# Performance work log

Measured on AMD Instinct MI355X. Metric: run time of the kernel, lower is better.

Reference implementation:

```python
import jax, jax.numpy as jnp
import numpy as np

B, T, D, H = 4, 2048, 1024, 16
DK, DV, CHUNK = D // H, 2 * D // H, 64  # head_k_dim=64, head_v_dim=128 (expand_v=2.0)
EPS = 1e-5


def setup_inputs() -> dict:
    key = jax.random.key(0)
    ks = jax.random.split(key, 6)
    s = 0.02
    return {
        "x": jax.random.normal(ks[0], (B, T, D), jnp.float32),
        "Wq": jax.random.normal(ks[1], (D, H * DK), jnp.float32) * s,
        "Wk": jax.random.normal(ks[2], (D, H * DK), jnp.float32) * s,
        "Wv": jax.random.normal(ks[3], (D, H * DV), jnp.float32) * s,
        "Wg": jax.random.normal(ks[4], (D, H * DV), jnp.float32) * s,
        "Wo": jax.random.normal(ks[5], (H * DV, D), jnp.float32) * s,
        "g_norm_w": jnp.ones((DV,), jnp.float32),
    }


def _rope(q):
    # q: [B, T, H, DK]; non-interleaved (rotate-half) rotary, base 10000
    half = DK // 2
    inv_freq = 1.0 / (10000.0 ** (jnp.arange(half, dtype=jnp.float32) / half))
    freqs = jnp.arange(T, dtype=jnp.float32)[:, None] * inv_freq  # [T, half]
    cos = jnp.cos(freqs)[None, :, None, :]
    sin = jnp.sin(freqs)[None, :, None, :]
    q1, q2 = q[..., :half], q[..., half:]
    return jnp.concatenate([q1 * cos - q2 * sin, q2 * cos + q1 * sin], axis=-1)


def reference(x, Wq, Wk, Wv, Wg, Wo, g_norm_w):
    q = _rope((x @ Wq).reshape(B, T, H, DK)) * (DK ** -0.5)
    k = _rope((x @ Wk).reshape(B, T, H, DK))
    v = (x @ Wv).reshape(B, T, H, DV)

    N = T // CHUNK
    def tochunks(t):  # [B,T,H,Dh] -> [N,B,H,C,Dh]
        return t.reshape(B, N, CHUNK, H, t.shape[-1]).transpose(1, 0, 3, 2, 4)
    qc, kc, vc = tochunks(q), tochunks(k), tochunks(v)

    # per-head RetNet decay: gamma_h = 1 - 2^{-5-h}
    gamma = 1.0 - jnp.exp2(-5.0 - jnp.arange(H, dtype=jnp.float32))  # [H]
    i = jnp.arange(CHUNK, dtype=jnp.float32)
    # intra-chunk decay mask D[h,i,j] = gamma^{i-j} for j<=i else 0
    Dmask = jnp.where(i[:, None] >= i[None, :],
                      gamma[:, None, None] ** (i[:, None] - i[None, :]), 0.0)  # [H,C,C]
    cross = gamma[:, None] ** (i + 1.0)          # [H,C] query decay vs prev state
    kdec = gamma[:, None] ** (CHUNK - 1.0 - i)   # [H,C] key decay into new state
    chunk_dec = gamma ** CHUNK                   # [H]

    def step(S, qkv):
        q_, k_, v_ = qkv  # [B,H,C,DK], [B,H,C,DK], [B,H,C,DV]
        attn = jnp.einsum('bhid,bhjd->bhij', q_, k_) * Dmask
        o = jnp.einsum('bhij,bhjv->bhiv', attn, v_)
        o = o + jnp.einsum('bhid,bhdv->bhiv', q_ * cross[None, :, :, None], S)
        S = S * chunk_dec[None, :, None, None] + \
            jnp.einsum('bhjd,bhjv->bhdv', k_ * kdec[None, :, :, None], v_)
        return S, o

    S0 = jnp.zeros((B, H, DK, DV), x.dtype)
    _, o = jax.lax.scan(step, S0, (qc, kc, vc))  # [N,B,H,C,DV]
    o = o.transpose(1, 0, 3, 2, 4).reshape(B, T, H, DV)

    # fused RMSNorm + swish gate (FusedRMSNormSwishGate)
    g = (x @ Wg).reshape(B, T, H, DV)
    o = o * jax.lax.rsqrt(jnp.mean(o * o, axis=-1, keepdims=True) + EPS) * g_norm_w
    o = o * (g * jax.nn.sigmoid(g))
    return o.reshape(B, T, H * DV) @ Wo
```

## Files before the change

kernel.cpp:

```cpp
#include <hip/hip_runtime.h>
#include <hip/hip_bf16.h>
#include <math.h>

typedef unsigned short u16;
typedef unsigned int u32;
typedef __attribute__((ext_vector_type(8))) short bf16x8;
typedef __attribute__((ext_vector_type(4))) float f32x4;


__device__ __forceinline__ u16 f2bf(float f) {
  union { float f; unsigned u; } a; a.f = f;
  unsigned u = a.u;
  unsigned r = (u + 0x7fffu + ((u >> 16) & 1u)) >> 16;
  return (u16)r;
}
__device__ __forceinline__ float bf2f(u16 s) {
  union { unsigned u; float f; } a; a.u = ((unsigned)s) << 16; return a.f;
}

__global__ void k_sentinel(float* out) {
  if (threadIdx.x == 0 && blockIdx.x == 0) out[0] = 1.0e6f;
}

__device__ __forceinline__ void split8r(const float* t, bf16x8& hi, bf16x8& lo) {
#pragma unroll
  for (int m = 0; m < 8; ++m) {
    union { float f; u32 u; } c; c.f = t[m];
    union { u32 u; float f; } hf; hf.u = c.u & 0xffff0000u;
    union { float f; u32 u; } lw; lw.f = t[m] - hf.f;
    hi[m] = (short)(u16)(c.u >> 16);
    lo[m] = (short)(u16)(lw.u >> 16);
  }
}
__device__ __forceinline__ void split8p(const float* __restrict__ p, bf16x8& hi, bf16x8& lo) {
  f32x4 a = *(const f32x4*)p;
  f32x4 b = *(const f32x4*)(p + 4);
  float t[8];
  t[0]=a[0]; t[1]=a[1]; t[2]=a[2]; t[3]=a[3]; t[4]=b[0]; t[5]=b[1]; t[6]=b[2]; t[7]=b[3];
  split8r(t, hi, lo);
}

__device__ __forceinline__ void bar_lds() {
  asm volatile("s_waitcnt lgkmcnt(0)" ::: "memory");
  __builtin_amdgcn_sched_barrier(0);
  __builtin_amdgcn_s_barrier();
}

__device__ __forceinline__ void gload16(const u16* g, u16* l) {
  __builtin_amdgcn_global_load_lds(
      (const __attribute__((address_space(1))) unsigned int*)g,
      (__attribute__((address_space(3))) unsigned int*)l, 16, 0, 0);
}

__global__ __launch_bounds__(256) void k_cvt_x(const float* __restrict__ src, u16* __restrict__ dst) {
  int i = blockIdx.x * 256 + threadIdx.x;
  float4 v = ((const float4*)src)[i];
  ushort4 o;
  o.x = f2bf(v.x); o.y = f2bf(v.y); o.z = f2bf(v.z); o.w = f2bf(v.w);
  ((ushort4*)dst)[i] = o;
}

__global__ __launch_bounds__(256) void k_ropetab(float2* __restrict__ tab) {
  int idx = blockIdx.x * 256 + threadIdx.x;
  int t = idx >> 5, i = idx & 31;
  float invf = powf(10000.f, -(float)i * (1.f / 32.f));
  float ang = (float)t * invf;
  float2 cs; cs.x = cosf(ang); cs.y = sinf(ang);
  tab[idx] = cs;
}

__global__ __launch_bounds__(256) void k_transpose_all(
    const float* __restrict__ Wq, const float* __restrict__ Wk, const float* __restrict__ Wv,
    const float* __restrict__ Wg, const float* __restrict__ Wo,
    u16* __restrict__ Wqkb, u16* __restrict__ Wvgb, u16* __restrict__ Wob) {
  int z = blockIdx.x;
  const float* src; u16* dst; int K, N, bx, by;
  if (z < 1024)      { src = Wq; dst = Wqkb;                       K = 1024; N = 1024; int r = z;        bx = r & 31; by = r >> 5; }
  else if (z < 2048) { src = Wk; dst = Wqkb + (size_t)1024 * 1024; K = 1024; N = 1024; int r = z - 1024; bx = r & 31; by = r >> 5; }
  else if (z < 4096) { src = Wv; dst = Wvgb;                       K = 1024; N = 2048; int r = z - 2048; bx = r & 63; by = r >> 6; }
  else if (z < 6144) { src = Wg; dst = Wvgb + (size_t)2048 * 1024; K = 1024; N = 2048; int r = z - 4096; bx = r & 63; by = r >> 6; }
  else               { src = Wo; dst = Wob;                        K = 2048; N = 1024; int r = z - 6144; bx = r & 31; by = r >> 5; }
  __shared__ float tile[32][33];
  int n0 = bx * 32, k0 = by * 32;
  int tx = threadIdx.x & 31, ty = threadIdx.x >> 5;
  for (int r = 0; r < 32; r += 8)
    tile[ty + r][tx] = src[(size_t)(k0 + ty + r) * N + n0 + tx];
  __syncthreads();
  for (int r = 0; r < 32; r += 8)
    dst[(size_t)(n0 + ty + r) * K + k0 + tx] = f2bf(tile[tx][ty + r]);
}

#define STG3(t, sl)                                                                  \
  {                                                                                  \
    _Pragma("unroll")                                                                \
    for (int q = 0; q < 2; ++q) {                                                    \
      int s = w * 2 + q;                                                             \
      int dByte = s * 1024 + lane * 16;                                              \
      int u = dByte ^ (((dByte >> 9) & 1) << 5);                                     \
      int row = u >> 6, cb = u & 63;                                                 \
      gload16(&A[(size_t)(i0 + row) * K + (t) * 32 + (cb >> 1)], &As[sl][s * 512]);  \
      gload16(&Bt[(size_t)(n0 + row) * K + (t) * 32 + (cb >> 1)], &Bs[sl][s * 512]); \
    }                                                                                \
  }

__global__ __launch_bounds__(256, 2) void k_gemm_qkvg(const u16* __restrict__ A, const u16* __restrict__ Bt,
                                                      float* __restrict__ qk, u16* __restrict__ vg,
                                                      const float2* __restrict__ tab, int K) {
  __shared__ __attribute__((aligned(16))) u16 As[3][128 * 32];
  __shared__ __attribute__((aligned(16))) u16 Bs[3][128 * 32];
  int id = blockIdx.y * 48 + blockIdx.x;
  int x = id & 7, loc = id >> 3;
  int bxg = loc / 48, rem = loc - bxg * 48;
  int by8 = rem / 6, bxi = rem - by8 * 6;
  int bx = bxg * 6 + bxi, by = x * 8 + by8;
  int i0 = by * 128, n0 = bx * 128;
  int tid = threadIdx.x;
  int lane = tid & 63, w = tid >> 6;
  int wr = (w >> 1) * 64, wc = (w & 1) * 64;
  f32x4 acc[4][4];
#pragma unroll
  for (int m = 0; m < 4; ++m)
#pragma unroll
    for (int n = 0; n < 4; ++n) acc[m][n] = (f32x4){0.f, 0.f, 0.f, 0.f};
  int fr = lane & 15, kq = lane >> 4;
  int nkt = K >> 5;

  STG3(0, 0);
  STG3(1, 1);
  for (int t = 0; t < nkt; ++t) {
    if (t < nkt - 1) asm volatile("s_waitcnt vmcnt(4)" ::: "memory");
    else             asm volatile("s_waitcnt vmcnt(0)" ::: "memory");
    asm volatile("s_waitcnt lgkmcnt(0)" ::: "memory");
    __builtin_amdgcn_sched_barrier(0);
    __builtin_amdgcn_s_barrier();
    if (t + 2 < nkt) STG3(t + 2, (t + 2) % 3);
    int cur = t % 3;
    bf16x8 af[4], bfr[4];
#pragma unroll
    for (int m = 0; m < 4; ++m) {
      int rr = wr + m * 16 + fr;
      int idx = (rr * 32 + kq * 8) ^ (((rr >> 3) & 1) << 4);
      af[m] = *(const bf16x8*)&As[cur][idx];
    }
#pragma unroll
    for (int n = 0; n < 4; ++n) {
      int rr = wc + n * 16 + fr;
      int idx = (rr * 32 + kq * 8) ^ (((rr >> 3) & 1) << 4);
      bfr[n] = *(const bf16x8*)&Bs[cur][idx];
    }
    __builtin_amdgcn_s_setprio(1);
#pragma unroll
    for (int m = 0; m < 4; ++m)
#pragma unroll
      for (int n = 0; n < 4; ++n)
        acc[m][n] = __builtin_amdgcn_mfma_f32_16x16x32_bf16(af[m], bfr[n], acc[m][n], 0, 0, 0);
    __builtin_amdgcn_s_setprio(0);
  }

  int rb = (lane >> 4) * 4, cb2 = lane & 15;
  if (n0 < 2048) {
    float scale = (n0 < 1024) ? 0.125f : 1.0f;
#pragma unroll
    for (int m = 0; m < 4; ++m)
#pragma unroll
      for (int n = 0; n < 2; ++n) {
        int gc = n0 + wc + n * 16 + cb2;
        int ii = n * 16 + cb2;
#pragma unroll
        for (int r = 0; r < 4; ++r) {
          int gr = i0 + wr + m * 16 + rb + r;
          int t = gr & 2047;
          float2 cs = tab[t * 32 + ii];
          float q1 = acc[m][n][r], q2 = acc[m][n + 2][r];
          qk[(size_t)gr * 2048 + gc]      = (q1 * cs.x - q2 * cs.y) * scale;
          qk[(size_t)gr * 2048 + gc + 32] = (q2 * cs.x + q1 * cs.y) * scale;
        }
      }
  } else {
#pragma unroll
    for (int m = 0; m < 4; ++m)
#pragma unroll
      for (int n = 0; n < 4; ++n) {
        int gr = i0 + wr + m * 16 + rb;
        int gc = n0 - 2048 + wc + n * 16 + cb2;
#pragma unroll
        for (int r = 0; r < 4; ++r)
          vg[(size_t)(gr + r) * 4096 + gc] = f2bf(acc[m][n][r]);
      }
  }
}

__global__ __launch_bounds__(256, 2) void k_gemm_out(const u16* __restrict__ A, const u16* __restrict__ Bt,
                                                     float* __restrict__ Cv, int N, int K) {
  __shared__ __attribute__((aligned(16))) u16 As[3][128 * 32];
  __shared__ __attribute__((aligned(16))) u16 Bs[3][128 * 32];
  int nbx = gridDim.x;
  int id = blockIdx.y * nbx + blockIdx.x;
  int cpx = (nbx * gridDim.y) >> 3;
  int sw = (id & 7) * cpx + (id >> 3);
  int bx = sw % nbx, by = sw / nbx;
  int i0 = by * 128, n0 = bx * 128;
  int tid = threadIdx.x;
  int lane = tid & 63, w = tid >> 6;
  int wr = (w >> 1) * 64, wc = (w & 1) * 64;
  f32x4 acc[4][4];
#pragma unroll
  for (int m = 0; m < 4; ++m)
#pragma unroll
    for (int n = 0; n < 4; ++n) acc[m][n] = (f32x4){0.f, 0.f, 0.f, 0.f};
  int fr = lane & 15, kq = lane >> 4;
  int nkt = K >> 5;

  STG3(0, 0);
  STG3(1, 1);
  for (int t = 0; t < nkt; ++t) {
    if (t < nkt - 1) asm volatile("s_waitcnt vmcnt(4)" ::: "memory");
    else             asm volatile("s_waitcnt vmcnt(0)" ::: "memory");
    asm volatile("s_waitcnt lgkmcnt(0)" ::: "memory");
    __builtin_amdgcn_sched_barrier(0);
    __builtin_amdgcn_s_barrier();
    if (t + 2 < nkt) STG3(t + 2, (t + 2) % 3);
    int cur = t % 3;
    bf16x8 af[4], bfr[4];
#pragma unroll
    for (int m = 0; m < 4; ++m) {
      int rr = wr + m * 16 + fr;
      int idx = (rr * 32 + kq * 8) ^ (((rr >> 3) & 1) << 4);
      af[m] = *(const bf16x8*)&As[cur][idx];
    }
#pragma unroll
    for (int n = 0; n < 4; ++n) {
      int rr = wc + n * 16 + fr;
      int idx = (rr * 32 + kq * 8) ^ (((rr >> 3) & 1) << 4);
      bfr[n] = *(const bf16x8*)&Bs[cur][idx];
    }
    __builtin_amdgcn_s_setprio(1);
#pragma unroll
    for (int m = 0; m < 4; ++m)
#pragma unroll
      for (int n = 0; n < 4; ++n)
        acc[m][n] = __builtin_amdgcn_mfma_f32_16x16x32_bf16(af[m], bfr[n], acc[m][n], 0, 0, 0);
    __builtin_amdgcn_s_setprio(0);
  }

  int rb = (lane >> 4) * 4, cb2 = lane & 15;
#pragma unroll
  for (int m = 0; m < 4; ++m)
#pragma unroll
    for (int n = 0; n < 4; ++n) {
      int gr = i0 + wr + m * 16 + rb;
      int gc = n0 + wc + n * 16 + cb2;
#pragma unroll
      for (int r = 0; r < 4; ++r)
        Cv[(size_t)(gr + r) * N + gc] = acc[m][n][r];
    }
}

__global__ __launch_bounds__(512) void k_retention(const float* __restrict__ qk, const u16* __restrict__ vg,
                                                   const float* __restrict__ gnw, u16* __restrict__ og) {
  int bh = blockIdx.x & 63, rq = blockIdx.x >> 6;
  int h = bh & 15, b = bh >> 4;
  int gi0 = rq * 16;

  __shared__ __attribute__((aligned(16))) float qs[16][68];
  __shared__ __attribute__((aligned(16))) float ks[64][68];
  __shared__ __attribute__((aligned(16))) u16 vst[128][88];
  __shared__ __attribute__((aligned(16))) u16 kta_h[8][520];
  __shared__ __attribute__((aligned(16))) u16 kta_l[8][520];
  __shared__ __attribute__((aligned(16))) u16 pa_h[16][68];
  __shared__ __attribute__((aligned(16))) u16 pa_l[16][68];
  __shared__ __attribute__((aligned(16))) u16 sst_h[8][1040];
  __shared__ __attribute__((aligned(16))) u16 sst_l[8][1040];
  __shared__ float dpow[72];
  __shared__ float ssred[8][16];

  int tid = threadIdx.x;
  int w = tid >> 6, l = tid & 63;
  int fr = l & 15, fq = l >> 4;
  float gamma = 1.f - exp2f(-5.f - (float)h);
  if (tid <= 64) dpow[tid] = powf(gamma, (float)tid);
  for (int c = tid; c < 4160; c += 512) { ((u32*)sst_h)[c] = 0; ((u32*)sst_l)[c] = 0; }
  __syncthreads();
  float cdec = dpow[64];

  int e0 = w * 16;
  float gww = gnw[e0 + fr];
  int khmax = (rq < 2) ? 1 : 2;

  int qi = tid >> 4, qd4 = (tid & 15) * 4;
  int sj = tid >> 3, sdg = (tid & 7) * 8;
  int vjp = tid & 31, ve8 = (tid >> 5) * 8;

  f32x4 Sacc[4][2];
#pragma unroll
  for (int dt = 0; dt < 4; ++dt)
#pragma unroll
    for (int nt = 0; nt < 2; ++nt) Sacc[dt][nt] = (f32x4){0.f, 0.f, 0.f, 0.f};

  f32x4 pq = (f32x4){0.f, 0.f, 0.f, 0.f};
  f32x4 pk0, pk1;
  bf16x8 pva, pvb;
  {
    int rowbase = b * 2048;
    if (tid < 256) pq = *(const f32x4*)&qk[(size_t)(rowbase + gi0 + qi) * 2048 + h * 64 + qd4];
    const float* kr = &qk[(size_t)(rowbase + sj) * 2048 + 1024 + h * 64 + sdg];
    pk0 = *(const f32x4*)kr;
    pk1 = *(const f32x4*)(kr + 4);
    const u16* vr = &vg[(size_t)(rowbase + 2 * vjp) * 4096 + h * 128 + ve8];
    pva = *(const bf16x8*)vr;
    pvb = *(const bf16x8*)(vr + 4096);
  }

  for (int n = 0; n < 32; ++n) {
    int rowbase = b * 2048 + n * 64;
    if (tid < 256) *(f32x4*)&qs[qi][qd4] = pq;
    {
      *(f32x4*)&ks[sj][sdg] = pk0;
      *(f32x4*)&ks[sj][sdg + 4] = pk1;
      float kdv = dpow[63 - sj];
      float kd[8];
#pragma unroll
      for (int m = 0; m < 4; ++m) { kd[m] = pk0[m] * kdv; kd[m + 4] = pk1[m] * kdv; }
      bf16x8 kh8, kl8;
      split8r(kd, kh8, kl8);
      int J = sj >> 3, s = sj & 7, dh = tid & 7;
#pragma unroll
      for (int m = 0; m < 8; ++m) {
        int blk = (dh * 8) | (m ^ dh);
        kta_h[J][blk * 8 + s] = (u16)kh8[m];
        kta_l[J][blk * 8 + s] = (u16)kl8[m];
      }
#pragma unroll
      for (int m = 0; m < 8; ++m)
        *(u32*)&vst[ve8 + m][2 * vjp] = (u32)(u16)pva[m] | ((u32)(u16)pvb[m] << 16);
    }
    __syncthreads();
    if (n < 31) {
      int rb2 = rowbase + 64;
      if (tid < 256) pq = *(const f32x4*)&qk[(size_t)(rb2 + gi0 + qi) * 2048 + h * 64 + qd4];
      const float* kr = &qk[(size_t)(rb2 + sj) * 2048 + 1024 + h * 64 + sdg];
      pk0 = *(const f32x4*)kr;
      pk1 = *(const f32x4*)(kr + 4);
      const u16* vr = &vg[(size_t)(rb2 + 2 * vjp) * 4096 + h * 128 + ve8];
      pva = *(const bf16x8*)vr;
      pvb = *(const bf16x8*)(vr + 4096);
    }
    bf16x8 qhc[2], qlc[2];
    split8p(&qs[fr][fq * 8], qhc[0], qlc[0]);
    split8p(&qs[fr][32 + fq * 8], qhc[1], qlc[1]);
    if (w < 4) {
      int ct = w;
      f32x4 at = (f32x4){0.f, 0.f, 0.f, 0.f};
      if (16 * ct <= gi0 + 15) {
#pragma unroll
        for (int kh = 0; kh < 2; ++kh) {
          bf16x8 kbh, kbl;
          split8p(&ks[16 * ct + fr][kh * 32 + fq * 8], kbh, kbl);
          at = __builtin_amdgcn_mfma_f32_16x16x32_bf16(kbh, qhc[kh], at, 0, 0, 0);
          at = __builtin_amdgcn_mfma_f32_16x16x32_bf16(kbl, qhc[kh], at, 0, 0, 0);
          at = __builtin_amdgcn_mfma_f32_16x16x32_bf16(kbh, qlc[kh], at, 0, 0, 0);
        }
      }
      int jb = 16 * ct + fq * 4;
      ushort4 wh, wl;
#pragma unroll
      for (int r = 0; r < 4; ++r) {
        int s = gi0 + fr - (jb + r);
        float val = (s >= 0) ? at[r] * dpow[s] : 0.f;
        union { float f; u32 u; } c; c.f = val;
        union { u32 u; float f; } hf; hf.u = c.u & 0xffff0000u;
        union { float f; u32 u; } lw; lw.f = val - hf.f;
        ((u16*)&wh)[r] = (u16)(c.u >> 16);
        ((u16*)&wl)[r] = (u16)(lw.u >> 16);
      }
      *(ushort4*)&pa_h[fr][jb] = wh;
      *(ushort4*)&pa_l[fr][jb] = wl;
    } else if (n < 31) {
      int eb = (w - 4) * 32;
#pragma unroll
      for (int dt = 0; dt < 4; ++dt)
#pragma unroll
        for (int nt = 0; nt < 2; ++nt)
#pragma unroll
          for (int r = 0; r < 4; ++r) Sacc[dt][nt][r] *= cdec;
      bf16x8 bv[2][2];
#pragma unroll
      for (int kh2 = 0; kh2 < 2; ++kh2)
#pragma unroll
        for (int nt = 0; nt < 2; ++nt)
          bv[kh2][nt] = *(const bf16x8*)&vst[eb + nt * 16 + fr][kh2 * 32 + fq * 8];
#pragma unroll
      for (int kh2 = 0; kh2 < 2; ++kh2) {
#pragma unroll
        for (int dt = 0; dt < 4; ++dt) {
          int d = dt * 16 + fr;
          int blk = d ^ ((dt * 2 + (fr >> 3)) & 7);
          bf16x8 ah = *(const bf16x8*)&kta_h[kh2 * 4 + fq][blk * 8];
          bf16x8 al = *(const bf16x8*)&kta_l[kh2 * 4 + fq][blk * 8];
#pragma unroll
          for (int nt = 0; nt < 2; ++nt) {
            Sacc[dt][nt] = __builtin_amdgcn_mfma_f32_16x16x32_bf16(ah, bv[kh2][nt], Sacc[dt][nt], 0, 0, 0);
            Sacc[dt][nt] = __builtin_amdgcn_mfma_f32_16x16x32_bf16(al, bv[kh2][nt], Sacc[dt][nt], 0, 0, 0);
          }
        }
      }
    }
    bar_lds();
    f32x4 o1 = (f32x4){0.f, 0.f, 0.f, 0.f};
    f32x4 o2 = (f32x4){0.f, 0.f, 0.f, 0.f};
#pragma unroll
    for (int kh2 = 0; kh2 < 2; ++kh2) {
      bf16x8 sh = *(const bf16x8*)&sst_h[kh2 * 4 + fq][(e0 + fr) * 8];
      bf16x8 sl = *(const bf16x8*)&sst_l[kh2 * 4 + fq][(e0 + fr) * 8];
      o2 = __builtin_amdgcn_mfma_f32_16x16x32_bf16(qhc[kh2], sh, o2, 0, 0, 0);
      o2 = __builtin_amdgcn_mfma_f32_16x16x32_bf16(qhc[kh2], sl, o2, 0, 0, 0);
      o2 = __builtin_amdgcn_mfma_f32_16x16x32_bf16(qlc[kh2], sh, o2, 0, 0, 0);
      if (kh2 < khmax) {
        bf16x8 ph = *(const bf16x8*)&pa_h[fr][kh2 * 32 + fq * 8];
        bf16x8 pl = *(const bf16x8*)&pa_l[fr][kh2 * 32 + fq * 8];
        bf16x8 bvv = *(const bf16x8*)&vst[e0 + fr][kh2 * 32 + fq * 8];
        o1 = __builtin_amdgcn_mfma_f32_16x16x32_bf16(ph, bvv, o1, 0, 0, 0);
        o1 = __builtin_amdgcn_mfma_f32_16x16x32_bf16(pl, bvv, o1, 0, 0, 0);
      }
    }
    float ofin[4], ssp[4];
#pragma unroll
    for (int r = 0; r < 4; ++r) {
      int gi = gi0 + fq * 4 + r;
      ofin[r] = o1[r] + dpow[gi + 1] * o2[r];
      ssp[r] = ofin[r] * ofin[r];
    }
#pragma unroll
    for (int r = 0; r < 4; ++r) {
      ssp[r] += __shfl_xor(ssp[r], 1, 64);
      ssp[r] += __shfl_xor(ssp[r], 2, 64);
      ssp[r] += __shfl_xor(ssp[r], 4, 64);
      ssp[r] += __shfl_xor(ssp[r], 8, 64);
    }
    if (fr == 0) {
#pragma unroll
      for (int r = 0; r < 4; ++r) ssred[w][fq * 4 + r] = ssp[r];
    }
    bar_lds();
#pragma unroll
    for (int r = 0; r < 4; ++r) {
      int i16 = fq * 4 + r;
      float tot = 0.f;
#pragma unroll
      for (int w2 = 0; w2 < 8; ++w2) tot += ssred[w2][i16];
      float rms = rsqrtf(tot * (1.f / 128.f) + 1e-5f);
      int grow = rowbase + gi0 + i16;
      float g = bf2f(vg[(size_t)grow * 4096 + 2048 + h * 128 + e0 + fr]);
      float y = ofin[r] * rms * gww * (g / (1.f + expf(-g)));
      og[(size_t)grow * 2048 + h * 128 + e0 + fr] = f2bf(y);
    }
    if (w >= 4 && n < 31) {
      int eb = (w - 4) * 32;
#pragma unroll
      for (int dt = 0; dt < 4; ++dt) {
        int g = dt * 2 + (fq >> 1);
#pragma unroll
        for (int nt = 0; nt < 2; ++nt) {
          int e = eb + nt * 16 + fr;
          ushort4 wh, wl;
#pragma unroll
          for (int r = 0; r < 4; ++r) {
            union { float f; u32 u; } c; c.f = Sacc[dt][nt][r];
            union { u32 u; float f; } hf; hf.u = c.u & 0xffff0000u;
            union { float f; u32 u; } lw; lw.f = Sacc[dt][nt][r] - hf.f;
            ((u16*)&wh)[r] = (u16)(c.u >> 16);
            ((u16*)&wl)[r] = (u16)(lw.u >> 16);
          }
          int idx = e * 8 + (fq & 1) * 4;
          *(ushort4*)&sst_h[g][idx] = wh;
          *(ushort4*)&sst_l[g][idx] = wl;
        }
      }
    }
  }
}

extern "C" void kernel_launch(void* const* d_in, const int* in_sizes, int n_in,
                              void* d_out, int out_size, void* d_ws, size_t ws_size,
                              hipStream_t stream) {
  const float* x   = (const float*)d_in[0];
  const float* Wq  = (const float*)d_in[1];
  const float* Wk  = (const float*)d_in[2];
  const float* Wv  = (const float*)d_in[3];
  const float* Wg  = (const float*)d_in[4];
  const float* Wo  = (const float*)d_in[5];
  const float* gnw = (const float*)d_in[6];
  float* out = (float*)d_out;

  const size_t MB = 1024 * 1024;
  char* ws = (char*)d_ws;
  u16*   xb   = (u16*)(ws + 0 * MB);
  u16*   Wqkb = (u16*)(ws + 16 * MB);
  u16*   Wvgb = (u16*)(ws + 20 * MB);
  float2* tab = (float2*)(ws + 28 * MB);
  float* qk   = (float*)(ws + 32 * MB);
  u16*   vg   = (u16*)(ws + 96 * MB);
  u16*   Wob  = (u16*)(ws + 160 * MB);
  u16*   og   = (u16*)(ws + 0 * MB);
  const size_t NEED = 164 * MB;
  if (ws_size < NEED) {
    k_sentinel<<<1, 64, 0, stream>>>(out);
    return;
  }

  k_cvt_x<<<8192, 256, 0, stream>>>(x, xb);
  k_ropetab<<<256, 256, 0, stream>>>(tab);
  k_transpose_all<<<8192, 256, 0, stream>>>(Wq, Wk, Wv, Wg, Wo, Wqkb, Wvgb, Wob);

  k_gemm_qkvg<<<dim3(48, 64), 256, 0, stream>>>(xb, Wqkb, qk, vg, tab, 1024);
  k_retention<<<256, 512, 0, stream>>>(qk, vg, gnw, og);
  k_gemm_out<<<dim3(8, 64), 256, 0, stream>>>(og, Wob, out, 1024, 2048);
}
```

Baseline: 299.9 us.

## Retention kernel: 32 query rows per block with 1024 threads

The retention kernel now has each block handle 32 query rows of a chunk instead of 16, using 1024 threads (16 waves), so the grid halves from 256 to 128 blocks. The per-chunk state update S is split across 8 waves instead of 4, each holding one 16-column tile, which cuts per-wave MFMA work and accumulator registers. Each block shares one K/V chunk load and one state update among twice as many query rows, reducing the redundant state recomputation that every query-row block does for each (b,h). The cost is fewer blocks than CUs on the GPU, larger blocks with more barrier contention, and per-lane Q splitting repeated inside the loops.

```diff
diff --git a/kernel.cpp b/kernel.cpp
--- a/kernel.cpp
+++ b/kernel.cpp
@@ -38,6 +38,16 @@
   float t[8];
   t[0]=a[0]; t[1]=a[1]; t[2]=a[2]; t[3]=a[3]; t[4]=b[0]; t[5]=b[1]; t[6]=b[2]; t[7]=b[3];
   split8r(t, hi, lo);
+}
+__device__ __forceinline__ void split4r(const float* t, u16* hi, u16* lo) {
+#pragma unroll
+  for (int m = 0; m < 4; ++m) {
+    union { float f; u32 u; } c; c.f = t[m];
+    union { u32 u; float f; } hf; hf.u = c.u & 0xffff0000u;
+    union { float f; u32 u; } lw; lw.f = t[m] - hf.f;
+    hi[m] = (u16)(c.u >> 16);
+    lo[m] = (u16)(lw.u >> 16);
+  }
 }
 
 __device__ __forceinline__ void bar_lds() {
@@ -256,116 +266,107 @@
     }
 }
 
-__global__ __launch_bounds__(512) void k_retention(const float* __restrict__ qk, const u16* __restrict__ vg,
-                                                   const float* __restrict__ gnw, u16* __restrict__ og) {
-  int bh = blockIdx.x & 63, rq = blockIdx.x >> 6;
+__global__ __launch_bounds__(1024, 4) void k_retention(const float* __restrict__ qk, const u16* __restrict__ vg,
+                                                       const float* __restrict__ gnw, u16* __restrict__ og) {
+  int bh = blockIdx.x & 63, mq = blockIdx.x >> 6;
   int h = bh & 15, b = bh >> 4;
-  int gi0 = rq * 16;
-
-  __shared__ __attribute__((aligned(16))) float qs[16][68];
+  int gi0 = mq * 32;
+
+  __shared__ __attribute__((aligned(16))) float qs[32][68];
   __shared__ __attribute__((aligned(16))) float ks[64][68];
   __shared__ __attribute__((aligned(16))) u16 vst[128][88];
   __shared__ __attribute__((aligned(16))) u16 kta_h[8][520];
   __shared__ __attribute__((aligned(16))) u16 kta_l[8][520];
-  __shared__ __attribute__((aligned(16))) u16 pa_h[16][68];
-  __shared__ __attribute__((aligned(16))) u16 pa_l[16][68];
+  __shared__ __attribute__((aligned(16))) u16 pa_h[32][72];
+  __shared__ __attribute__((aligned(16))) u16 pa_l[32][72];
   __shared__ __attribute__((aligned(16))) u16 sst_h[8][1040];
   __shared__ __attribute__((aligned(16))) u16 sst_l[8][1040];
   __shared__ float dpow[72];
-  __shared__ float ssred[8][16];
+  __shared__ float ssred[16][16];
 
   int tid = threadIdx.x;
   int w = tid >> 6, l = tid & 63;
   int fr = l & 15, fq = l >> 4;
   float gamma = 1.f - exp2f(-5.f - (float)h);
   if (tid <= 64) dpow[tid] = powf(gamma, (float)tid);
-  for (int c = tid; c < 4160; c += 512) { ((u32*)sst_h)[c] = 0; ((u32*)sst_l)[c] = 0; }
+  for (int c = tid; c < 4160; c += 1024) { ((u32*)sst_h)[c] = 0; ((u32*)sst_l)[c] = 0; }
   __syncthreads();
   float cdec = dpow[64];
 
-  int e0 = w * 16;
-  float gww = gnw[e0 + fr];
-  int khmax = (rq < 2) ? 1 : 2;
+  int orh = w >> 3, oes = (w & 7) * 16;
+  int arh = (w >> 2) & 1, act = w & 3;
+  int es = (w & 7) * 16;
+  float gww = gnw[oes + fr];
+  int khmax = (mq == 0) ? 1 : 2;
 
   int qi = tid >> 4, qd4 = (tid & 15) * 4;
-  int sj = tid >> 3, sdg = (tid & 7) * 8;
-  int vjp = tid & 31, ve8 = (tid >> 5) * 8;
-
-  f32x4 Sacc[4][2];
-#pragma unroll
-  for (int dt = 0; dt < 4; ++dt)
-#pragma unroll
-    for (int nt = 0; nt < 2; ++nt) Sacc[dt][nt] = (f32x4){0.f, 0.f, 0.f, 0.f};
+  int sj = tid >> 4, dq = tid & 15;
+  int jp = tid & 31, ve4 = (tid >> 5) * 4;
+
+  f32x4 Sacc[4];
+#pragma unroll
+  for (int dt = 0; dt < 4; ++dt) Sacc[dt] = (f32x4){0.f, 0.f, 0.f, 0.f};
 
   f32x4 pq = (f32x4){0.f, 0.f, 0.f, 0.f};
-  f32x4 pk0, pk1;
-  bf16x8 pva, pvb;
+  f32x4 pk;
+  ushort4 pva, pvb;
   {
     int rowbase = b * 2048;
-    if (tid < 256) pq = *(const f32x4*)&qk[(size_t)(rowbase + gi0 + qi) * 2048 + h * 64 + qd4];
-    const float* kr = &qk[(size_t)(rowbase + sj) * 2048 + 1024 + h * 64 + sdg];
-    pk0 = *(const f32x4*)kr;
-    pk1 = *(const f32x4*)(kr + 4);
-    const u16* vr = &vg[(size_t)(rowbase + 2 * vjp) * 4096 + h * 128 + ve8];
-    pva = *(const bf16x8*)vr;
-    pvb = *(const bf16x8*)(vr + 4096);
+    if (tid < 512) pq = *(const f32x4*)&qk[(size_t)(rowbase + gi0 + qi) * 2048 + h * 64 + qd4];
+    pk = *(const f32x4*)&qk[(size_t)(rowbase + sj) * 2048 + 1024 + h * 64 + dq * 4];
+    pva = *(const ushort4*)&vg[(size_t)(rowbase + 2 * jp) * 4096 + h * 128 + ve4];
+    pvb = *(const ushort4*)&vg[(size_t)(rowbase + 2 * jp + 1) * 4096 + h * 128 + ve4];
   }
 
   for (int n = 0; n < 32; ++n) {
     int rowbase = b * 2048 + n * 64;
-    if (tid < 256) *(f32x4*)&qs[qi][qd4] = pq;
+    if (tid < 512) *(f32x4*)&qs[qi][qd4] = pq;
     {
-      *(f32x4*)&ks[sj][sdg] = pk0;
-      *(f32x4*)&ks[sj][sdg + 4] = pk1;
+      *(f32x4*)&ks[sj][dq * 4] = pk;
       float kdv = dpow[63 - sj];
-      float kd[8];
-#pragma unroll
-      for (int m = 0; m < 4; ++m) { kd[m] = pk0[m] * kdv; kd[m + 4] = pk1[m] * kdv; }
-      bf16x8 kh8, kl8;
-      split8r(kd, kh8, kl8);
-      int J = sj >> 3, s = sj & 7, dh = tid & 7;
-#pragma unroll
-      for (int m = 0; m < 8; ++m) {
-        int blk = (dh * 8) | (m ^ dh);
-        kta_h[J][blk * 8 + s] = (u16)kh8[m];
-        kta_l[J][blk * 8 + s] = (u16)kl8[m];
-      }
-#pragma unroll
-      for (int m = 0; m < 8; ++m)
-        *(u32*)&vst[ve8 + m][2 * vjp] = (u32)(u16)pva[m] | ((u32)(u16)pvb[m] << 16);
+      float kd[4];
+#pragma unroll
+      for (int m = 0; m < 4; ++m) kd[m] = pk[m] * kdv;
+      u16 kh4[4], kl4[4];
+      split4r(kd, kh4, kl4);
+      int J = sj >> 3, s = sj & 7, dh = dq >> 1;
+#pragma unroll
+      for (int m = 0; m < 4; ++m) {
+        int dl = (dq & 1) * 4 + m;
+        int blk = (dh * 8) | (dl ^ dh);
+        kta_h[J][blk * 8 + s] = kh4[m];
+        kta_l[J][blk * 8 + s] = kl4[m];
+      }
+#pragma unroll
+      for (int m = 0; m < 4; ++m)
+        *(u32*)&vst[ve4 + m][2 * jp] = (u32)((u16*)&pva)[m] | ((u32)((u16*)&pvb)[m] << 16);
     }
     __syncthreads();
     if (n < 31) {
       int rb2 = rowbase + 64;
-      if (tid < 256) pq = *(const f32x4*)&qk[(size_t)(rb2 + gi0 + qi) * 2048 + h * 64 + qd4];
-      const float* kr = &qk[(size_t)(rb2 + sj) * 2048 + 1024 + h * 64 + sdg];
-      pk0 = *(const f32x4*)kr;
-      pk1 = *(const f32x4*)(kr + 4);
-      const u16* vr = &vg[(size_t)(rb2 + 2 * vjp) * 4096 + h * 128 + ve8];
-      pva = *(const bf16x8*)vr;
-      pvb = *(const bf16x8*)(vr + 4096);
-    }
-    bf16x8 qhc[2], qlc[2];
-    split8p(&qs[fr][fq * 8], qhc[0], qlc[0]);
-    split8p(&qs[fr][32 + fq * 8], qhc[1], qlc[1]);
-    if (w < 4) {
-      int ct = w;
+      if (tid < 512) pq = *(const f32x4*)&qk[(size_t)(rb2 + gi0 + qi) * 2048 + h * 64 + qd4];
+      pk = *(const f32x4*)&qk[(size_t)(rb2 + sj) * 2048 + 1024 + h * 64 + dq * 4];
+      pva = *(const ushort4*)&vg[(size_t)(rb2 + 2 * jp) * 4096 + h * 128 + ve4];
+      pvb = *(const ushort4*)&vg[(size_t)(rb2 + 2 * jp + 1) * 4096 + h * 128 + ve4];
+    }
+    if (w < 8) {
       f32x4 at = (f32x4){0.f, 0.f, 0.f, 0.f};
-      if (16 * ct <= gi0 + 15) {
+      if (16 * act <= gi0 + arh * 16 + 15) {
 #pragma unroll
         for (int kh = 0; kh < 2; ++kh) {
-          bf16x8 kbh, kbl;
-          split8p(&ks[16 * ct + fr][kh * 32 + fq * 8], kbh, kbl);
-          at = __builtin_amdgcn_mfma_f32_16x16x32_bf16(kbh, qhc[kh], at, 0, 0, 0);
-          at = __builtin_amdgcn_mfma_f32_16x16x32_bf16(kbl, qhc[kh], at, 0, 0, 0);
-          at = __builtin_amdgcn_mfma_f32_16x16x32_bf16(kbh, qlc[kh], at, 0, 0, 0);
+          bf16x8 qh, ql, kbh, kbl;
+          split8p(&qs[arh * 16 + fr][kh * 32 + fq * 8], qh, ql);
+          split8p(&ks[16 * act + fr][kh * 32 + fq * 8], kbh, kbl);
+          at = __builtin_amdgcn_mfma_f32_16x16x32_bf16(kbh, qh, at, 0, 0, 0);
+          at = __builtin_amdgcn_mfma_f32_16x16x32_bf16(kbl, qh, at, 0, 0, 0);
+          at = __builtin_amdgcn_mfma_f32_16x16x32_bf16(kbh, ql, at, 0, 0, 0);
         }
       }
-      int jb = 16 * ct + fq * 4;
+      int jb = 16 * act + fq * 4;
       ushort4 wh, wl;
 #pragma unroll
       for (int r = 0; r < 4; ++r) {
-        int s = gi0 + fr - (jb + r);
+        int s = gi0 + arh * 16 + fr - (jb + r);
         float val = (s >= 0) ? at[r] * dpow[s] : 0.f;
         union { float f; u32 u; } c; c.f = val;
         union { u32 u; float f; } hf; hf.u = c.u & 0xffff0000u;
@@ -373,22 +374,17 @@
         ((u16*)&wh)[r] = (u16)(c.u >> 16);
         ((u16*)&wl)[r] = (u16)(lw.u >> 16);
       }
-      *(ushort4*)&pa_h[fr][jb] = wh;
-      *(ushort4*)&pa_l[fr][jb] = wl;
+      *(ushort4*)&pa_h[arh * 16 + fr][jb] = wh;
+      *(ushort4*)&pa_l[arh * 16 + fr][jb] = wl;
     } else if (n < 31) {
-      int eb = (w - 4) * 32;
 #pragma unroll
       for (int dt = 0; dt < 4; ++dt)
 #pragma unroll
-        for (int nt = 0; nt < 2; ++nt)
-#pragma unroll
-          for (int r = 0; r < 4; ++r) Sacc[dt][nt][r] *= cdec;
-      bf16x8 bv[2][2];
+        for (int r = 0; r < 4; ++r) Sacc[dt][r] *= cdec;
+      bf16x8 bv[2];
 #pragma unroll
       for (int kh2 = 0; kh2 < 2; ++kh2)
-#pragma unroll
-        for (int nt = 0; nt < 2; ++nt)
-          bv[kh2][nt] = *(const bf16x8*)&vst[eb + nt * 16 + fr][kh2 * 32 + fq * 8];
+        bv[kh2] = *(const bf16x8*)&vst[es + fr][kh2 * 32 + fq * 8];
 #pragma unroll
       for (int kh2 = 0; kh2 < 2; ++kh2) {
 #pragma unroll
@@ -397,11 +393,8 @@
           int blk = d ^ ((dt * 2 + (fr >> 3)) & 7);
           bf16x8 ah = *(const bf16x8*)&kta_h[kh2 * 4 + fq][blk * 8];
           bf16x8 al = *(const bf16x8*)&kta_l[kh2 * 4 + fq][blk * 8];
-#pragma unroll
-          for (int nt = 0; nt < 2; ++nt) {
-            Sacc[dt][nt] = __builtin_amdgcn_mfma_f32_16x16x32_bf16(ah, bv[kh2][nt], Sacc[dt][nt], 0, 0, 0);
-            Sacc[dt][nt] = __builtin_amdgcn_mfma_f32_16x16x32_bf16(al, bv[kh2][nt], Sacc[dt][nt], 0, 0, 0);
-          }
+          Sacc[dt] = __builtin_amdgcn_mfma_f32_16x16x32_bf16(ah, bv[kh2], Sacc[dt], 0, 0, 0);
+          Sacc[dt] = __builtin_amdgcn_mfma_f32_16x16x32_bf16(al, bv[kh2], Sacc[dt], 0, 0, 0);
         }
       }
     }
@@ -410,15 +403,17 @@
     f32x4 o2 = (f32x4){0.f, 0.f, 0.f, 0.f};
 #pragma unroll
     for (int kh2 = 0; kh2 < 2; ++kh2) {
-      bf16x8 sh = *(const bf16x8*)&sst_h[kh2 * 4 + fq][(e0 + fr) * 8];
-      bf16x8 sl = *(const bf16x8*)&sst_l[kh2 * 4 + fq][(e0 + fr) * 8];
-      o2 = __builtin_amdgcn_mfma_f32_16x16x32_bf16(qhc[kh2], sh, o2, 0, 0, 0);
-      o2 = __builtin_amdgcn_mfma_f32_16x16x32_bf16(qhc[kh2], sl, o2, 0, 0, 0);
-      o2 = __builtin_amdgcn_mfma_f32_16x16x32_bf16(qlc[kh2], sh, o2, 0, 0, 0);
+      bf16x8 qh, ql;
+      split8p(&qs[orh * 16 + fr][kh2 * 32 + fq * 8], qh, ql);
+      bf16x8 sh = *(const bf16x8*)&sst_h[kh2 * 4 + fq][(oes + fr) * 8];
+      bf16x8 sl = *(const bf16x8*)&sst_l[kh2 * 4 + fq][(oes + fr) * 8];
+      o2 = __builtin_amdgcn_mfma_f32_16x16x32_bf16(qh, sh, o2, 0, 0, 0);
+      o2 = __builtin_amdgcn_mfma_f32_16x16x32_bf16(qh, sl, o2, 0, 0, 0);
+      o2 = __builtin_amdgcn_mfma_f32_16x16x32_bf16(ql, sh, o2, 0, 0, 0);
       if (kh2 < khmax) {
-        bf16x8 ph = *(const bf16x8*)&pa_h[fr][kh2 * 32 + fq * 8];
-        bf16x8 pl = *(const bf16x8*)&pa_l[fr][kh2 * 32 + fq * 8];
-        bf16x8 bvv = *(const bf16x8*)&vst[e0 + fr][kh2 * 32 + fq * 8];
+        bf16x8 ph = *(const bf16x8*)&pa_h[orh * 16 + fr][kh2 * 32 + fq * 8];
+        bf16x8 pl = *(const bf16x8*)&pa_l[orh * 16 + fr][kh2 * 32 + fq * 8];
+        bf16x8 bvv = *(const bf16x8*)&vst[oes + fr][kh2 * 32 + fq * 8];
         o1 = __builtin_amdgcn_mfma_f32_16x16x32_bf16(ph, bvv, o1, 0, 0, 0);
         o1 = __builtin_amdgcn_mfma_f32_16x16x32_bf16(pl, bvv, o1, 0, 0, 0);
       }
@@ -426,7 +421,7 @@
     float ofin[4], ssp[4];
 #pragma unroll
     for (int r = 0; r < 4; ++r) {
-      int gi = gi0 + fq * 4 + r;
+      int gi = gi0 + orh * 16 + fq * 4 + r;
       ofin[r] = o1[r] + dpow[gi + 1] * o2[r];
       ssp[r] = ofin[r] * ofin[r];
     }
@@ -447,34 +442,30 @@
       int i16 = fq * 4 + r;
       float tot = 0.f;
 #pragma unroll
-      for (int w2 = 0; w2 < 8; ++w2) tot += ssred[w2][i16];
+      for (int w2 = 0; w2 < 8; ++w2) tot += ssred[orh * 8 + w2][i16];
       float rms = rsqrtf(tot * (1.f / 128.f) + 1e-5f);
-      int grow = rowbase + gi0 + i16;
-      float g = bf2f(vg[(size_t)grow * 4096 + 2048 + h * 128 + e0 + fr]);
+      int grow = rowbase + gi0 + orh * 16 + i16;
+      float g = bf2f(vg[(size_t)grow * 4096 + 2048 + h * 128 + oes + fr]);
       float y = ofin[r] * rms * gww * (g / (1.f + expf(-g)));
-      og[(size_t)grow * 2048 + h * 128 + e0 + fr] = f2bf(y);
-    }
-    if (w >= 4 && n < 31) {
-      int eb = (w - 4) * 32;
+      og[(size_t)grow * 2048 + h * 128 + oes + fr] = f2bf(y);
+    }
+    if (w >= 8 && n < 31) {
 #pragma unroll
       for (int dt = 0; dt < 4; ++dt) {
-        int g = dt * 2 + (fq >> 1);
-#pragma unroll
-        for (int nt = 0; nt < 2; ++nt) {
-          int e = eb + nt * 16 + fr;
-          ushort4 wh, wl;
-#pragma unroll
-          for (int r = 0; r < 4; ++r) {
-            union { float f; u32 u; } c; c.f = Sacc[dt][nt][r];
-            union { u32 u; float f; } hf; hf.u = c.u & 0xffff0000u;
-            union { float f; u32 u; } lw; lw.f = Sacc[dt][nt][r] - hf.f;
-            ((u16*)&wh)[r] = (u16)(c.u >> 16);
-            ((u16*)&wl)[r] = (u16)(lw.u >> 16);
-          }
-          int idx = e * 8 + (fq & 1) * 4;
-          *(ushort4*)&sst_h[g][idx] = wh;
-          *(ushort4*)&sst_l[g][idx] = wl;
+        int g2 = dt * 2 + (fq >> 1);
+        int e = es + fr;
+        ushort4 wh, wl;
+#pragma unroll
+        for (int r = 0; r < 4; ++r) {
+          union { float f; u32 u; } c; c.f = Sacc[dt][r];
+          union { u32 u; float f; } hf; hf.u = c.u & 0xffff0000u;
+          union { float f; u32 u; } lw; lw.f = Sacc[dt][r] - hf.f;
+          ((u16*)&wh)[r] = (u16)(c.u >> 16);
+          ((u16*)&wl)[r] = (u16)(lw.u >> 16);
         }
+        int idx = e * 8 + (fq & 1) * 4;
+        *(ushort4*)&sst_h[g2][idx] = wh;
+        *(ushort4*)&sst_l[g2][idx] = wl;
       }
     }
   }
@@ -513,6 +504,6 @@
   k_transpose_all<<<8192, 256, 0, stream>>>(Wq, Wk, Wv, Wg, Wo, Wqkb, Wvgb, Wob);
 
   k_gemm_qkvg<<<dim3(48, 64), 256, 0, stream>>>(xb, Wqkb, qk, vg, tab, 1024);
-  k_retention<<<256, 512, 0, stream>>>(qk, vg, gnw, og);
+  k_retention<<<128, 1024, 0, stream>>>(qk, vg, gnw, og);
   k_gemm_out<<<dim3(8, 64), 256, 0, stream>>>(og, Wob, out, 1024, 2048);
 }
```

Measured after the change: 385.6 us. 1.29x slower.

## Switch GEMM pipelines to double-buffered 64-wide K tiles with one barrier per tile

Applied to the files above, without the earlier changes.

Both bf16 GEMM kernels change from a 3-stage ring of 32-wide K tiles to a 2-stage double buffer of 64-wide K tiles (two 32-wide sub-tiles each). Each iteration issues the next tile's async global-to-LDS loads, runs MFMAs over both sub-tiles, then waits for all loads and hits a single barrier. This halves the number of barriers and loop iterations per GEMM. In exchange, prefetch depth drops to one tile ahead and the loop waits on vmcnt(0) at every step, which may expose more memory latency. LDS use rises from 48KB to 64KB per block, which could affect the two-blocks-per-CU occupancy.

```diff
diff --git a/kernel.cpp b/kernel.cpp
--- a/kernel.cpp
+++ b/kernel.cpp
@@ -42,6 +42,12 @@
 
 __device__ __forceinline__ void bar_lds() {
   asm volatile("s_waitcnt lgkmcnt(0)" ::: "memory");
+  __builtin_amdgcn_sched_barrier(0);
+  __builtin_amdgcn_s_barrier();
+}
+
+__device__ __forceinline__ void bar_vm() {
+  asm volatile("s_waitcnt vmcnt(0)" ::: "memory");
   __builtin_amdgcn_sched_barrier(0);
   __builtin_amdgcn_s_barrier();
 }
@@ -90,24 +96,29 @@
     dst[(size_t)(n0 + ty + r) * K + k0 + tx] = f2bf(tile[tx][ty + r]);
 }
 
-#define STG3(t, sl)                                                                  \
-  {                                                                                  \
-    _Pragma("unroll")                                                                \
-    for (int q = 0; q < 2; ++q) {                                                    \
-      int s = w * 2 + q;                                                             \
-      int dByte = s * 1024 + lane * 16;                                              \
-      int u = dByte ^ (((dByte >> 9) & 1) << 5);                                     \
-      int row = u >> 6, cb = u & 63;                                                 \
-      gload16(&A[(size_t)(i0 + row) * K + (t) * 32 + (cb >> 1)], &As[sl][s * 512]);  \
-      gload16(&Bt[(size_t)(n0 + row) * K + (t) * 32 + (cb >> 1)], &Bs[sl][s * 512]); \
-    }                                                                                \
+#define STG64(t, sl)                                                                   \
+  {                                                                                    \
+    _Pragma("unroll")                                                                  \
+    for (int kk = 0; kk < 2; ++kk) {                                                   \
+      _Pragma("unroll")                                                                \
+      for (int q = 0; q < 2; ++q) {                                                    \
+        int s = w * 2 + q;                                                             \
+        int dByte = s * 1024 + lane * 16;                                              \
+        int u = dByte ^ (((dByte >> 9) & 1) << 5);                                     \
+        int row = u >> 6, cb = u & 63;                                                 \
+        gload16(&A[(size_t)(i0 + row) * K + (t) * 64 + kk * 32 + (cb >> 1)],           \
+                &As[sl][kk][s * 512]);                                                 \
+        gload16(&Bt[(size_t)(n0 + row) * K + (t) * 64 + kk * 32 + (cb >> 1)],          \
+                &Bs[sl][kk][s * 512]);                                                 \
+      }                                                                                \
+    }                                                                                  \
   }
 
 __global__ __launch_bounds__(256, 2) void k_gemm_qkvg(const u16* __restrict__ A, const u16* __restrict__ Bt,
                                                       float* __restrict__ qk, u16* __restrict__ vg,
                                                       const float2* __restrict__ tab, int K) {
-  __shared__ __attribute__((aligned(16))) u16 As[3][128 * 32];
-  __shared__ __attribute__((aligned(16))) u16 Bs[3][128 * 32];
+  __shared__ __attribute__((aligned(16))) u16 As[2][2][128 * 32];
+  __shared__ __attribute__((aligned(16))) u16 Bs[2][2][128 * 32];
   int id = blockIdx.y * 48 + blockIdx.x;
   int x = id & 7, loc = id >> 3;
   int bxg = loc / 48, rem = loc - bxg * 48;
@@ -123,38 +134,37 @@
 #pragma unroll
     for (int n = 0; n < 4; ++n) acc[m][n] = (f32x4){0.f, 0.f, 0.f, 0.f};
   int fr = lane & 15, kq = lane >> 4;
-  int nkt = K >> 5;
-
-  STG3(0, 0);
-  STG3(1, 1);
+  int nkt = K >> 6;
+
+  STG64(0, 0);
+  bar_vm();
   for (int t = 0; t < nkt; ++t) {
-    if (t < nkt - 1) asm volatile("s_waitcnt vmcnt(4)" ::: "memory");
-    else             asm volatile("s_waitcnt vmcnt(0)" ::: "memory");
-    asm volatile("s_waitcnt lgkmcnt(0)" ::: "memory");
-    __builtin_amdgcn_sched_barrier(0);
-    __builtin_amdgcn_s_barrier();
-    if (t + 2 < nkt) STG3(t + 2, (t + 2) % 3);
-    int cur = t % 3;
-    bf16x8 af[4], bfr[4];
-#pragma unroll
-    for (int m = 0; m < 4; ++m) {
-      int rr = wr + m * 16 + fr;
-      int idx = (rr * 32 + kq * 8) ^ (((rr >> 3) & 1) << 4);
-      af[m] = *(const bf16x8*)&As[cur][idx];
-    }
-#pragma unroll
-    for (int n = 0; n < 4; ++n) {
-      int rr = wc + n * 16 + fr;
-      int idx = (rr * 32 + kq * 8) ^ (((rr >> 3) & 1) << 4);
-      bfr[n] = *(const bf16x8*)&Bs[cur][idx];
-    }
-    __builtin_amdgcn_s_setprio(1);
-#pragma unroll
-    for (int m = 0; m < 4; ++m)
-#pragma unroll
-      for (int n = 0; n < 4; ++n)
-        acc[m][n] = __builtin_amdgcn_mfma_f32_16x16x32_bf16(af[m], bfr[n], acc[m][n], 0, 0, 0);
-    __builtin_amdgcn_s_setprio(0);
+    int sl = t & 1;
+    if (t + 1 < nkt) STG64(t + 1, sl ^ 1);
+#pragma unroll
+    for (int kk = 0; kk < 2; ++kk) {
+      bf16x8 af[4], bfr[4];
+#pragma unroll
+      for (int m = 0; m < 4; ++m) {
+        int rr = wr + m * 16 + fr;
+        int idx = (rr * 32 + kq * 8) ^ (((rr >> 3) & 1) << 4);
+        af[m] = *(const bf16x8*)&As[sl][kk][idx];
+      }
+#pragma unroll
+      for (int n = 0; n < 4; ++n) {
+        int rr = wc + n * 16 + fr;
+        int idx = (rr * 32 + kq * 8) ^ (((rr >> 3) & 1) << 4);
+        bfr[n] = *(const bf16x8*)&Bs[sl][kk][idx];
+      }
+      __builtin_amdgcn_s_setprio(1);
+#pragma unroll
+      for (int m = 0; m < 4; ++m)
+#pragma unroll
+        for (int n = 0; n < 4; ++n)
+          acc[m][n] = __builtin_amdgcn_mfma_f32_16x16x32_bf16(af[m], bfr[n], acc[m][n], 0, 0, 0);
+      __builtin_amdgcn_s_setprio(0);
+    }
+    bar_vm();
   }
 
   int rb = (lane >> 4) * 4, cb2 = lane & 15;
@@ -192,8 +202,8 @@
 
 __global__ __launch_bounds__(256, 2) void k_gemm_out(const u16* __restrict__ A, const u16* __restrict__ Bt,
                                                      float* __restrict__ Cv, int N, int K) {
-  __shared__ __attribute__((aligned(16))) u16 As[3][128 * 32];
-  __shared__ __attribute__((aligned(16))) u16 Bs[3][128 * 32];
+  __shared__ __attribute__((aligned(16))) u16 As[2][2][128 * 32];
+  __shared__ __attribute__((aligned(16))) u16 Bs[2][2][128 * 32];
   int nbx = gridDim.x;
   int id = blockIdx.y * nbx + blockIdx.x;
   int cpx = (nbx * gridDim.y) >> 3;
@@ -209,38 +219,37 @@
 #pragma unroll
     for (int n = 0; n < 4; ++n) acc[m][n] = (f32x4){0.f, 0.f, 0.f, 0.f};
   int fr = lane & 15, kq = lane >> 4;
-  int nkt = K >> 5;
-
-  STG3(0, 0);
-  STG3(1, 1);
+  int nkt = K >> 6;
+
+  STG64(0, 0);
+  bar_vm();
   for (int t = 0; t < nkt; ++t) {
-    if (t < nkt - 1) asm volatile("s_waitcnt vmcnt(4)" ::: "memory");
-    else             asm volatile("s_waitcnt vmcnt(0)" ::: "memory");
-    asm volatile("s_waitcnt lgkmcnt(0)" ::: "memory");
-    __builtin_amdgcn_sched_barrier(0);
-    __builtin_amdgcn_s_barrier();
-    if (t + 2 < nkt) STG3(t + 2, (t + 2) % 3);
-    int cur = t % 3;
-    bf16x8 af[4], bfr[4];
-#pragma unroll
-    for (int m = 0; m < 4; ++m) {
-      int rr = wr + m * 16 + fr;
-      int idx = (rr * 32 + kq * 8) ^ (((rr >> 3) & 1) << 4);
-      af[m] = *(const bf16x8*)&As[cur][idx];
-    }
-#pragma unroll
-    for (int n = 0; n < 4; ++n) {
-      int rr = wc + n * 16 + fr;
-      int idx = (rr * 32 + kq * 8) ^ (((rr >> 3) & 1) << 4);
-      bfr[n] = *(const bf16x8*)&Bs[cur][idx];
-    }
-    __builtin_amdgcn_s_setprio(1);
-#pragma unroll
-    for (int m = 0; m < 4; ++m)
-#pragma unroll
-      for (int n = 0; n < 4; ++n)
-        acc[m][n] = __builtin_amdgcn_mfma_f32_16x16x32_bf16(af[m], bfr[n], acc[m][n], 0, 0, 0);
-    __builtin_amdgcn_s_setprio(0);
+    int sl = t & 1;
+    if (t + 1 < nkt) STG64(t + 1, sl ^ 1);
+#pragma unroll
+    for (int kk = 0; kk < 2; ++kk) {
+      bf16x8 af[4], bfr[4];
+#pragma unroll
+      for (int m = 0; m < 4; ++m) {
+        int rr = wr + m * 16 + fr;
+        int idx = (rr * 32 + kq * 8) ^ (((rr >> 3) & 1) << 4);
+        af[m] = *(const bf16x8*)&As[sl][kk][idx];
+      }
+#pragma unroll
+      for (int n = 0; n < 4; ++n) {
+        int rr = wc + n * 16 + fr;
+        int idx = (rr * 32 + kq * 8) ^ (((rr >> 3) & 1) << 4);
+        bfr[n] = *(const bf16x8*)&Bs[sl][kk][idx];
+      }
+      __builtin_amdgcn_s_setprio(1);
+#pragma unroll
+      for (int m = 0; m < 4; ++m)
+#pragma unroll
+        for (int n = 0; n < 4; ++n)
+          acc[m][n] = __builtin_amdgcn_mfma_f32_16x16x32_bf16(af[m], bfr[n], acc[m][n], 0, 0, 0);
+      __builtin_amdgcn_s_setprio(0);
+    }
+    bar_vm();
   }
 
   int rb = (lane >> 4) * 4, cb2 = lane & 15;
```

After: 288.9 us. 1.04x faster.
